# Optimization experiments

Hardware: AMD Instinct MI355X
Metric: run time of the kernel (lower is better)

Reference implementation:

```python
import jax, jax.numpy as jnp
import numpy as np

N, B, C, H = 1024, 4, 1024, 8
D = C // H  # head dim = 128


def setup_inputs() -> dict:
    key = jax.random.key(0)
    ks = jax.random.split(key, 10)
    f = lambda k, s: jax.random.normal(k, s, dtype=jnp.float32)
    w = lambda k: f(k, (C, C)) * 0.02  # torch Linear weight layout (out, in)
    return {
        "query_reg": f(ks[0], (N, B, C)),
        "key_reg": f(ks[1], (N, B, C)),
        "query_cls": f(ks[2], (N, B, C)),
        "key_cls": f(ks[3], (N, B, C)),
        "value": f(ks[4], (N, B, C)),
        "W_q_reg": w(ks[5]),
        "W_k_reg": w(ks[6]),
        "W_q_cls": w(ks[7]),
        "W_k_cls": w(ks[8]),
        "W_v": w(ks[9]),
    }


def _proj_heads(x, W):
    # x: (N, B, C); torch Linear: y = x @ W.T -> reshape (N,B,H,D) -> (B,H,N,D)
    y = jnp.einsum('nbc,dc->nbd', x, W)
    return y.reshape(N, B, H, D).transpose(1, 2, 0, 3)


def _l2norm(x):
    return x / jnp.linalg.norm(x, axis=-1, keepdims=True)


def reference(query_reg, key_reg, query_cls, key_cls, value,
              W_q_reg, W_k_reg, W_q_cls, W_k_cls, W_v):
    q_reg = _l2norm(_proj_heads(query_reg, W_q_reg))  # (B,H,N,D)
    k_reg = _l2norm(_proj_heads(key_reg, W_k_reg))
    q_cls = _l2norm(_proj_heads(query_cls, W_q_cls))
    k_cls = _l2norm(_proj_heads(key_cls, W_k_cls))
    v = _proj_heads(value, W_v)

    attn_reg = jax.nn.softmax(jnp.einsum('bhnd,bhmd->bhnm', q_reg, k_reg), axis=-1)
    attn_cls = jax.nn.softmax(jnp.einsum('bhnd,bhmd->bhnm', q_cls, k_cls), axis=-1)
    attn = (attn_reg + attn_cls) * 0.5  # (B,H,N,N)

    x = jnp.einsum('bhnm,bhmd->bhnd', attn, v)  # (B,H,N,D)
    x = x.transpose(0, 2, 1, 3).reshape(B, N, C)  # (B,N,C)
    return (x.transpose(1, 0, 2), attn)  # ((N,B,C), (B,H,N,N))
```

## Files before the change

### kernel.cpp

```cpp
#include <hip/hip_runtime.h>

#define DEVINL __device__ __forceinline__

typedef unsigned short u16;
typedef float f32x4 __attribute__((ext_vector_type(4)));
typedef __bf16 bf16x8 __attribute__((ext_vector_type(8)));

constexpr int N_ = 1024, B_ = 4, C_ = 1024, H_ = 8, D_ = 128;
constexpr int NB = N_ * B_;
constexpr int BH = B_ * H_;

DEVINL u16 f2bf(float f) {
  unsigned u = __builtin_bit_cast(unsigned, f);
  u += 0x7fffu + ((u >> 16) & 1u);
  return (u16)(u >> 16);
}
DEVINL float bf2f(u16 v) { return __builtin_bit_cast(float, ((unsigned)v) << 16); }

typedef __attribute__((address_space(1))) void gv_t;
typedef __attribute__((address_space(3))) void lv_t;
DEVINL void gload16(const void* g, void* l) {
  __builtin_amdgcn_global_load_lds((gv_t*)(unsigned long long)g,
                                   (lv_t*)(unsigned)(unsigned long long)l, 16, 0, 0);
}
DEVINL bf16x8 ld_frag(const u16* p) { return *(const bf16x8*)p; }
DEVINL f32x4 mfma16(bf16x8 a, bf16x8 b, f32x4 c) {
  return __builtin_amdgcn_mfma_f32_16x16x32_bf16(a, b, c, 0, 0, 0);
}

struct ConvArgs { const float* s[10]; u16* d[10]; int n[10]; };

__global__ __launch_bounds__(256) void k_convert(ConvArgs a) {
  const int which = blockIdx.y;
  const int i = (blockIdx.x * 256 + threadIdx.x) * 8;
  if (i >= a.n[which]) return;
  const float* s = a.s[which] + i;
  float4 v0 = *(const float4*)s;
  float4 v1 = *(const float4*)(s + 4);
  union { uint4 v; u16 r[8]; } u;
  u.r[0] = f2bf(v0.x); u.r[1] = f2bf(v0.y); u.r[2] = f2bf(v0.z); u.r[3] = f2bf(v0.w);
  u.r[4] = f2bf(v1.x); u.r[5] = f2bf(v1.y); u.r[6] = f2bf(v1.z); u.r[7] = f2bf(v1.w);
  *(uint4*)(a.d[which] + i) = u.v;
}

struct ProjArgs { const u16* X[5]; const u16* W[5]; u16* O[5]; };

__global__ __launch_bounds__(256) void k_proj(ProjArgs a) {
  __shared__ u16 lA[128 * 64];
  __shared__ u16 lB[128 * 64];
  __shared__ float lred[128][2];
  const int tid = threadIdx.x, w = tid >> 6, lane = tid & 63;
  const int qd = lane >> 4, m16 = lane & 15;
  const int wr = w >> 1, wc = w & 1;
  const int r0 = blockIdx.y * 128, d0 = blockIdx.x * 128;
  const u16* __restrict__ X = a.X[blockIdx.z];
  const u16* __restrict__ W = a.W[blockIdx.z];
  u16* __restrict__ O = a.O[blockIdx.z];
  const bool donorm = blockIdx.z < 4;

  f32x4 acc[4][4];
  const f32x4 fz = {0.f, 0.f, 0.f, 0.f};
#pragma unroll
  for (int i = 0; i < 4; ++i)
#pragma unroll
    for (int j = 0; j < 4; ++j) acc[i][j] = fz;

  for (int k0 = 0; k0 < C_; k0 += 64) {
    __syncthreads();
#pragma unroll
    for (int i = 0; i < 4; ++i) {
      int p = i * 256 + tid, row = p >> 3, cp = p & 7, cl = cp ^ (row & 7);
      gload16(X + (size_t)(r0 + row) * C_ + k0 + cl * 8, &lA[p * 8]);
    }
#pragma unroll
    for (int i = 0; i < 4; ++i) {
      int p = i * 256 + tid, row = p >> 3, cp = p & 7, cl = cp ^ (row & 7);
      gload16(W + (size_t)(d0 + row) * C_ + k0 + cl * 8, &lB[p * 8]);
    }
    __syncthreads();
#pragma unroll
    for (int ks = 0; ks < 2; ++ks) {
      bf16x8 af[4], bfr[4];
#pragma unroll
      for (int t = 0; t < 4; ++t) {
        int row = wr * 64 + t * 16 + m16;
        af[t] = ld_frag(&lA[row * 64 + (((ks * 4 + qd) ^ (row & 7)) * 8)]);
        int col = wc * 64 + t * 16 + m16;
        bfr[t] = ld_frag(&lB[col * 64 + (((ks * 4 + qd) ^ (col & 7)) * 8)]);
      }
#pragma unroll
      for (int rt = 0; rt < 4; ++rt)
#pragma unroll
        for (int ct = 0; ct < 4; ++ct)
          acc[rt][ct] = mfma16(af[rt], bfr[ct], acc[rt][ct]);
    }
  }
  if (donorm) {
    float s[4][4];
#pragma unroll
    for (int rt = 0; rt < 4; ++rt)
#pragma unroll
      for (int rg = 0; rg < 4; ++rg) {
        float t = 0.f;
#pragma unroll
        for (int ct = 0; ct < 4; ++ct) t += acc[rt][ct][rg] * acc[rt][ct][rg];
        s[rt][rg] = t;
      }
#pragma unroll
    for (int off = 1; off < 16; off <<= 1)
#pragma unroll
      for (int rt = 0; rt < 4; ++rt)
#pragma unroll
        for (int rg = 0; rg < 4; ++rg) s[rt][rg] += __shfl_xor(s[rt][rg], off);
    if (m16 == 0) {
#pragma unroll
      for (int rt = 0; rt < 4; ++rt)
#pragma unroll
        for (int rg = 0; rg < 4; ++rg)
          lred[wr * 64 + rt * 16 + qd * 4 + rg][wc] = s[rt][rg];
    }
  }
  __syncthreads();
  float inv[4][4];
#pragma unroll
  for (int rt = 0; rt < 4; ++rt)
#pragma unroll
    for (int rg = 0; rg < 4; ++rg) {
      if (donorm) {
        int row = wr * 64 + rt * 16 + qd * 4 + rg;
        inv[rt][rg] = rsqrtf(lred[row][0] + lred[row][1]);
      } else inv[rt][rg] = 1.0f;
    }
#pragma unroll
  for (int rt = 0; rt < 4; ++rt)
#pragma unroll
    for (int ct = 0; ct < 4; ++ct)
#pragma unroll
      for (int rg = 0; rg < 4; ++rg) {
        int row = r0 + wr * 64 + rt * 16 + qd * 4 + rg;
        int col = d0 + wc * 64 + ct * 16 + m16;
        int n = row >> 2, b = row & 3, h = col >> 7, d = col & 127;
        O[(((size_t)(b * H_ + h)) * N_ + n) * D_ + d] = f2bf(acc[rt][ct][rg] * inv[rt][rg]);
      }
}

__global__ __launch_bounds__(256) void k_transpose(const u16* __restrict__ v,
                                                   u16* __restrict__ vt) {
  __shared__ u16 tile[128][65];
  const int bh = blockIdx.y, n0 = blockIdx.x * 64;
  const u16* src = v + (size_t)bh * N_ * D_;
  u16* dst = vt + (size_t)bh * D_ * N_;
  union U8 { uint4 v; u16 s[8]; };
#pragma unroll
  for (int it = 0; it < 4; ++it) {
    int c = it * 256 + threadIdx.x;
    int n = c >> 4, dc = (c & 15) * 8;
    U8 u; u.v = *(const uint4*)(src + (size_t)(n0 + n) * D_ + dc);
#pragma unroll
    for (int j = 0; j < 8; ++j) tile[dc + j][n] = u.s[j];
  }
  __syncthreads();
#pragma unroll
  for (int it = 0; it < 4; ++it) {
    int c = it * 256 + threadIdx.x;
    int d = c >> 3, nc = (c & 7) * 8;
    U8 u;
#pragma unroll
    for (int j = 0; j < 8; ++j) u.s[j] = tile[d][nc + j];
    *(uint4*)(dst + (size_t)d * N_ + n0 + nc) = u.v;
  }
}

__global__ __launch_bounds__(256, 2) void k_attn(const u16* __restrict__ qr,
                                                 const u16* __restrict__ kr,
                                                 const u16* __restrict__ qc,
                                                 const u16* __restrict__ kc,
                                                 const u16* __restrict__ vt,
                                                 float* __restrict__ out0,
                                                 float* __restrict__ out1) {
  __shared__ u16 lK[2][128 * 128];
  __shared__ u16 lP[32 * 136];
  __shared__ float lred[2][4][32];
  const int flat = blockIdx.x + (blockIdx.y << 5);
  const int xcd = flat & 7, kk = flat >> 3;
  const int bh = (xcd << 2) + (kk >> 5);
  const int n0 = (kk & 31) * 32;
  const int b = bh >> 3, h = bh & 7;
  const size_t base = (size_t)bh * N_ * D_;
  const int tid = threadIdx.x, w = tid >> 6, lane = tid & 63;
  const int qd = lane >> 4, m16 = lane & 15;

  bf16x8 qf[2][2][4];
#pragma unroll
  for (int ct = 0; ct < 2; ++ct)
#pragma unroll
    for (int ks = 0; ks < 4; ++ks) {
      size_t ro = base + (size_t)(n0 + ct * 16 + m16) * D_ + ks * 32 + qd * 8;
      qf[0][ct][ks] = ld_frag(qr + ro);
      qf[1][ct][ks] = ld_frag(qc + ro);
    }

  uint2 pst[2][8][2][2];
  float psum[2][2] = {{0.f, 0.f}, {0.f, 0.f}};
  const f32x4 fz = {0.f, 0.f, 0.f, 0.f};

#pragma unroll
  for (int mt = 0; mt < 8; ++mt) {
    const int m0 = mt * 128;
    __syncthreads();
#pragma unroll
    for (int i = 0; i < 8; ++i) {
      int p = i * 256 + tid, row = p >> 4, cp = p & 15, cl = cp ^ (row & 15);
      gload16(kr + base + (size_t)(m0 + row) * D_ + cl * 8, &lK[0][p * 8]);
    }
#pragma unroll
    for (int i = 0; i < 8; ++i) {
      int p = i * 256 + tid, row = p >> 4, cp = p & 15, cl = cp ^ (row & 15);
      gload16(kc + base + (size_t)(m0 + row) * D_ + cl * 8, &lK[1][p * 8]);
    }
    __syncthreads();
#pragma unroll
    for (int ty = 0; ty < 2; ++ty) {
#pragma unroll
      for (int rt = 0; rt < 2; ++rt) {
        bf16x8 af[4];
        const int mrow = w * 32 + rt * 16 + m16;
#pragma unroll
        for (int ks = 0; ks < 4; ++ks)
          af[ks] = ld_frag(&lK[ty][mrow * 128 + (((ks * 4 + qd) ^ (mrow & 15)) * 8)]);
#pragma unroll
        for (int ct = 0; ct < 2; ++ct) {
          f32x4 acc = fz;
#pragma unroll
          for (int ks = 0; ks < 4; ++ks) acc = mfma16(af[ks], qf[ty][ct][ks], acc);
          union { uint2 u; u16 s[4]; } pk;
          float loc = 0.f;
#pragma unroll
          for (int rg = 0; rg < 4; ++rg) {
            float e = __expf(acc[rg]);
            loc += e;
            pk.s[rg] = f2bf(e);
          }
          psum[ty][ct] += loc;
          pst[ty][mt][rt][ct] = pk.u;
        }
      }
    }
  }

#pragma unroll
  for (int ty = 0; ty < 2; ++ty)
#pragma unroll
    for (int ct = 0; ct < 2; ++ct) {
      psum[ty][ct] += __shfl_xor(psum[ty][ct], 16);
      psum[ty][ct] += __shfl_xor(psum[ty][ct], 32);
    }
  if (qd == 0) {
#pragma unroll
    for (int ty = 0; ty < 2; ++ty)
#pragma unroll
      for (int ct = 0; ct < 2; ++ct) lred[ty][w][ct * 16 + m16] = psum[ty][ct];
  }
  __syncthreads();
  float il[2][2];
#pragma unroll
  for (int ty = 0; ty < 2; ++ty)
#pragma unroll
    for (int ct = 0; ct < 2; ++ct) {
      int n = ct * 16 + m16;
      il[ty][ct] = 0.5f / (lred[ty][0][n] + lred[ty][1][n] + lred[ty][2][n] + lred[ty][3][n]);
    }

  f32x4 xacc[2][2];
#pragma unroll
  for (int ct = 0; ct < 2; ++ct)
#pragma unroll
    for (int dt = 0; dt < 2; ++dt) xacc[ct][dt] = fz;

  float* attn = out1 + (size_t)bh * N_ * N_;
  const u16* vtb = vt + (size_t)bh * D_ * N_;

#pragma unroll
  for (int mt = 0; mt < 8; ++mt) {
    const int m0 = mt * 128;
    __syncthreads();
#pragma unroll
    for (int rt = 0; rt < 2; ++rt)
#pragma unroll
      for (int ct = 0; ct < 2; ++ct) {
        union { uint2 u; u16 s[4]; } ur, uc, pk;
        ur.u = pst[0][mt][rt][ct];
        uc.u = pst[1][mt][rt][ct];
        f32x4 pv;
#pragma unroll
        for (int rg = 0; rg < 4; ++rg) {
          pv[rg] = bf2f(ur.s[rg]) * il[0][ct] + bf2f(uc.s[rg]) * il[1][ct];
          pk.s[rg] = f2bf(pv[rg]);
        }
        const int nrow = n0 + ct * 16 + m16;
        const int mcol = m0 + w * 32 + rt * 16 + qd * 4;
        *(f32x4*)(attn + (size_t)nrow * N_ + mcol) = pv;
        *(uint2*)&lP[(ct * 16 + m16) * 136 + w * 32 + rt * 16 + qd * 4] = pk.u;
      }
    __syncthreads();
#pragma unroll
    for (int ks = 0; ks < 4; ++ks) {
      bf16x8 pa[2], vb[2];
#pragma unroll
      for (int ct = 0; ct < 2; ++ct)
        pa[ct] = ld_frag(&lP[(ct * 16 + m16) * 136 + ks * 32 + qd * 8]);
#pragma unroll
      for (int dt = 0; dt < 2; ++dt)
        vb[dt] = ld_frag(vtb + (size_t)(w * 32 + dt * 16 + m16) * N_ + m0 + ks * 32 + qd * 8);
#pragma unroll
      for (int ct = 0; ct < 2; ++ct)
#pragma unroll
        for (int dt = 0; dt < 2; ++dt)
          xacc[ct][dt] = mfma16(pa[ct], vb[dt], xacc[ct][dt]);
    }
  }
#pragma unroll
  for (int ct = 0; ct < 2; ++ct)
#pragma unroll
    for (int dt = 0; dt < 2; ++dt)
#pragma unroll
      for (int rg = 0; rg < 4; ++rg) {
        int n = n0 + ct * 16 + qd * 4 + rg;
        int d = w * 32 + dt * 16 + m16;
        out0[((size_t)n * B_ + b) * C_ + h * 128 + d] = xacc[ct][dt][rg];
      }
}

extern "C" void kernel_launch(void* const* d_in, const int* in_sizes, int n_in,
                              void* d_out, int out_size, void* d_ws, size_t ws_size,
                              hipStream_t stream) {
  (void)in_sizes; (void)n_in; (void)out_size; (void)ws_size;
  const float* in_f[10];
  for (int i = 0; i < 10; ++i) in_f[i] = (const float*)d_in[i];

  u16* ws = (u16*)d_ws;
  u16* Xc[5], *Wc[5], *P[5];
  for (int i = 0; i < 5; ++i) Xc[i] = ws + (size_t)i * NB * C_;
  u16* wbase = ws + (size_t)5 * NB * C_;
  for (int i = 0; i < 5; ++i) Wc[i] = wbase + (size_t)i * C_ * C_;
  u16* pbase = wbase + (size_t)5 * C_ * C_;
  for (int i = 0; i < 5; ++i) P[i] = pbase + (size_t)i * BH * N_ * D_;
  u16* vt = pbase + (size_t)5 * BH * N_ * D_;

  float* out0 = (float*)d_out;
  float* out1 = out0 + (size_t)N_ * B_ * C_;

  ConvArgs ca;
  for (int i = 0; i < 5; ++i) { ca.s[i] = in_f[i];     ca.d[i] = Xc[i];  ca.n[i] = NB * C_; }
  for (int i = 0; i < 5; ++i) { ca.s[5+i] = in_f[5+i]; ca.d[5+i] = Wc[i]; ca.n[5+i] = C_ * C_; }
  k_convert<<<dim3(2048, 10), 256, 0, stream>>>(ca);

  ProjArgs pa;
  for (int i = 0; i < 5; ++i) { pa.X[i] = Xc[i]; pa.W[i] = Wc[i]; pa.O[i] = P[i]; }
  k_proj<<<dim3(C_ / 128, NB / 128, 5), 256, 0, stream>>>(pa);

  k_transpose<<<dim3(N_ / 64, BH), 256, 0, stream>>>(P[4], vt);

  k_attn<<<dim3(N_ / 32, BH), 256, 0, stream>>>(P[0], P[1], P[2], P[3], vt, out0, out1);
}
```

Baseline: 411.9 us.

## Double-buffer K tiles and widen attention block to eight waves

The attention kernel now runs 512 threads per block, so each wave handles 16 key rows or 16 head dims instead of 32. The next K tile is prefetched into a second LDS buffer while the current one is used for QK^T, and the P staging buffer is also doubled, which drops one barrier per iteration in the PV loop. The aim is to hide K load latency behind MFMA and exp work and to cut per-thread register pressure. The cost is roughly 145KB of LDS, which limits residency to one block per CU despite the launch bound of two.

```diff
diff --git a/kernel.cpp b/kernel.cpp
--- a/kernel.cpp
+++ b/kernel.cpp
@@ -171,16 +171,16 @@
   }
 }
 
-__global__ __launch_bounds__(256, 2) void k_attn(const u16* __restrict__ qr,
+__global__ __launch_bounds__(512, 2) void k_attn(const u16* __restrict__ qr,
                                                  const u16* __restrict__ kr,
                                                  const u16* __restrict__ qc,
                                                  const u16* __restrict__ kc,
                                                  const u16* __restrict__ vt,
                                                  float* __restrict__ out0,
                                                  float* __restrict__ out1) {
-  __shared__ u16 lK[2][128 * 128];
-  __shared__ u16 lP[32 * 136];
-  __shared__ float lred[2][4][32];
+  __shared__ u16 lK[2][2][128 * 128];
+  __shared__ u16 lP[2][32 * 136];
+  __shared__ float lred[2][8][32];
   const int flat = blockIdx.x + (blockIdx.y << 5);
   const int xcd = flat & 7, kk = flat >> 3;
   const int bh = (xcd << 2) + (kk >> 5);
@@ -189,6 +189,7 @@
   const size_t base = (size_t)bh * N_ * D_;
   const int tid = threadIdx.x, w = tid >> 6, lane = tid & 63;
   const int qd = lane >> 4, m16 = lane & 15;
+  const u16* ksrc[2] = {kr, kc};
 
   bf16x8 qf[2][2][4];
 #pragma unroll
@@ -200,52 +201,58 @@
       qf[1][ct][ks] = ld_frag(qc + ro);
     }
 
-  uint2 pst[2][8][2][2];
+  uint2 pst[2][8][2];
   float psum[2][2] = {{0.f, 0.f}, {0.f, 0.f}};
   const f32x4 fz = {0.f, 0.f, 0.f, 0.f};
 
 #pragma unroll
+  for (int ty = 0; ty < 2; ++ty)
+#pragma unroll
+    for (int i = 0; i < 4; ++i) {
+      int p = i * 512 + tid, row = p >> 4, cp = p & 15, cl = cp ^ (row & 15);
+      gload16(ksrc[ty] + base + (size_t)row * D_ + cl * 8, &lK[0][ty][p * 8]);
+    }
+  __syncthreads();
+
+#pragma unroll
   for (int mt = 0; mt < 8; ++mt) {
-    const int m0 = mt * 128;
+    const int cur = mt & 1;
+    if (mt < 7) {
+      const int m0n = (mt + 1) * 128;
+#pragma unroll
+      for (int ty = 0; ty < 2; ++ty)
+#pragma unroll
+        for (int i = 0; i < 4; ++i) {
+          int p = i * 512 + tid, row = p >> 4, cp = p & 15, cl = cp ^ (row & 15);
+          gload16(ksrc[ty] + base + (size_t)(m0n + row) * D_ + cl * 8,
+                  &lK[cur ^ 1][ty][p * 8]);
+        }
+    }
+    const int mrow = w * 16 + m16;
+#pragma unroll
+    for (int ty = 0; ty < 2; ++ty) {
+      bf16x8 af[4];
+#pragma unroll
+      for (int ks = 0; ks < 4; ++ks)
+        af[ks] = ld_frag(&lK[cur][ty][mrow * 128 + (((ks * 4 + qd) ^ (mrow & 15)) * 8)]);
+#pragma unroll
+      for (int ct = 0; ct < 2; ++ct) {
+        f32x4 acc = fz;
+#pragma unroll
+        for (int ks = 0; ks < 4; ++ks) acc = mfma16(af[ks], qf[ty][ct][ks], acc);
+        union { uint2 u; u16 s[4]; } pk;
+        float loc = 0.f;
+#pragma unroll
+        for (int rg = 0; rg < 4; ++rg) {
+          float e = __expf(acc[rg]);
+          loc += e;
+          pk.s[rg] = f2bf(e);
+        }
+        psum[ty][ct] += loc;
+        pst[ty][mt][ct] = pk.u;
+      }
+    }
     __syncthreads();
-#pragma unroll
-    for (int i = 0; i < 8; ++i) {
-      int p = i * 256 + tid, row = p >> 4, cp = p & 15, cl = cp ^ (row & 15);
-      gload16(kr + base + (size_t)(m0 + row) * D_ + cl * 8, &lK[0][p * 8]);
-    }
-#pragma unroll
-    for (int i = 0; i < 8; ++i) {
-      int p = i * 256 + tid, row = p >> 4, cp = p & 15, cl = cp ^ (row & 15);
-      gload16(kc + base + (size_t)(m0 + row) * D_ + cl * 8, &lK[1][p * 8]);
-    }
-    __syncthreads();
-#pragma unroll
-    for (int ty = 0; ty < 2; ++ty) {
-#pragma unroll
-      for (int rt = 0; rt < 2; ++rt) {
-        bf16x8 af[4];
-        const int mrow = w * 32 + rt * 16 + m16;
-#pragma unroll
-        for (int ks = 0; ks < 4; ++ks)
-          af[ks] = ld_frag(&lK[ty][mrow * 128 + (((ks * 4 + qd) ^ (mrow & 15)) * 8)]);
-#pragma unroll
-        for (int ct = 0; ct < 2; ++ct) {
-          f32x4 acc = fz;
-#pragma unroll
-          for (int ks = 0; ks < 4; ++ks) acc = mfma16(af[ks], qf[ty][ct][ks], acc);
-          union { uint2 u; u16 s[4]; } pk;
-          float loc = 0.f;
-#pragma unroll
-          for (int rg = 0; rg < 4; ++rg) {
-            float e = __expf(acc[rg]);
-            loc += e;
-            pk.s[rg] = f2bf(e);
-          }
-          psum[ty][ct] += loc;
-          pst[ty][mt][rt][ct] = pk.u;
-        }
-      }
-    }
   }
 
 #pragma unroll
@@ -268,67 +275,57 @@
 #pragma unroll
     for (int ct = 0; ct < 2; ++ct) {
       int n = ct * 16 + m16;
-      il[ty][ct] = 0.5f / (lred[ty][0][n] + lred[ty][1][n] + lred[ty][2][n] + lred[ty][3][n]);
-    }
-
-  f32x4 xacc[2][2];
+      float s = 0.f;
+#pragma unroll
+      for (int ww = 0; ww < 8; ++ww) s += lred[ty][ww][n];
+      il[ty][ct] = 0.5f / s;
+    }
+
+  f32x4 xacc[2] = {fz, fz};
+  float* attn = out1 + (size_t)bh * N_ * N_;
+  const u16* vtb = vt + (size_t)bh * D_ * N_ + (size_t)(w * 16 + m16) * N_;
+
+#pragma unroll
+  for (int mt = 0; mt < 8; ++mt) {
+    const int cur = mt & 1;
+    const int m0 = mt * 128;
+#pragma unroll
+    for (int ct = 0; ct < 2; ++ct) {
+      union { uint2 u; u16 s[4]; } ur, uc, pk;
+      ur.u = pst[0][mt][ct];
+      uc.u = pst[1][mt][ct];
+      f32x4 pv;
+#pragma unroll
+      for (int rg = 0; rg < 4; ++rg) {
+        pv[rg] = bf2f(ur.s[rg]) * il[0][ct] + bf2f(uc.s[rg]) * il[1][ct];
+        pk.s[rg] = f2bf(pv[rg]);
+      }
+      const int nrow = n0 + ct * 16 + m16;
+      const int mcol = m0 + w * 16 + qd * 4;
+      *(f32x4*)(attn + (size_t)nrow * N_ + mcol) = pv;
+      *(uint2*)&lP[cur][(ct * 16 + m16) * 136 + w * 16 + qd * 4] = pk.u;
+    }
+    __syncthreads();
+#pragma unroll
+    for (int ks = 0; ks < 4; ++ks) {
+      bf16x8 pa[2];
+#pragma unroll
+      for (int ct = 0; ct < 2; ++ct)
+        pa[ct] = ld_frag(&lP[cur][(ct * 16 + m16) * 136 + ks * 32 + qd * 8]);
+      bf16x8 vb = ld_frag(vtb + m0 + ks * 32 + qd * 8);
+#pragma unroll
+      for (int ct = 0; ct < 2; ++ct)
+        xacc[ct] = mfma16(pa[ct], vb, xacc[ct]);
+    }
+  }
 #pragma unroll
   for (int ct = 0; ct < 2; ++ct)
 #pragma unroll
-    for (int dt = 0; dt < 2; ++dt) xacc[ct][dt] = fz;
-
-  float* attn = out1 + (size_t)bh * N_ * N_;
-  const u16* vtb = vt + (size_t)bh * D_ * N_;
-
-#pragma unroll
-  for (int mt = 0; mt < 8; ++mt) {
-    const int m0 = mt * 128;
-    __syncthreads();
-#pragma unroll
-    for (int rt = 0; rt < 2; ++rt)
-#pragma unroll
-      for (int ct = 0; ct < 2; ++ct) {
-        union { uint2 u; u16 s[4]; } ur, uc, pk;
-        ur.u = pst[0][mt][rt][ct];
-        uc.u = pst[1][mt][rt][ct];
-        f32x4 pv;
-#pragma unroll
-        for (int rg = 0; rg < 4; ++rg) {
-          pv[rg] = bf2f(ur.s[rg]) * il[0][ct] + bf2f(uc.s[rg]) * il[1][ct];
-          pk.s[rg] = f2bf(pv[rg]);
-        }
-        const int nrow = n0 + ct * 16 + m16;
-        const int mcol = m0 + w * 32 + rt * 16 + qd * 4;
-        *(f32x4*)(attn + (size_t)nrow * N_ + mcol) = pv;
-        *(uint2*)&lP[(ct * 16 + m16) * 136 + w * 32 + rt * 16 + qd * 4] = pk.u;
-      }
-    __syncthreads();
-#pragma unroll
-    for (int ks = 0; ks < 4; ++ks) {
-      bf16x8 pa[2], vb[2];
-#pragma unroll
-      for (int ct = 0; ct < 2; ++ct)
-        pa[ct] = ld_frag(&lP[(ct * 16 + m16) * 136 + ks * 32 + qd * 8]);
-#pragma unroll
-      for (int dt = 0; dt < 2; ++dt)
-        vb[dt] = ld_frag(vtb + (size_t)(w * 32 + dt * 16 + m16) * N_ + m0 + ks * 32 + qd * 8);
-#pragma unroll
-      for (int ct = 0; ct < 2; ++ct)
-#pragma unroll
-        for (int dt = 0; dt < 2; ++dt)
-          xacc[ct][dt] = mfma16(pa[ct], vb[dt], xacc[ct][dt]);
-    }
-  }
-#pragma unroll
-  for (int ct = 0; ct < 2; ++ct)
-#pragma unroll
-    for (int dt = 0; dt < 2; ++dt)
-#pragma unroll
-      for (int rg = 0; rg < 4; ++rg) {
-        int n = n0 + ct * 16 + qd * 4 + rg;
-        int d = w * 32 + dt * 16 + m16;
-        out0[((size_t)n * B_ + b) * C_ + h * 128 + d] = xacc[ct][dt][rg];
-      }
+    for (int rg = 0; rg < 4; ++rg) {
+      int n = n0 + ct * 16 + qd * 4 + rg;
+      int d = w * 16 + m16;
+      out0[((size_t)n * B_ + b) * C_ + h * 128 + d] = xacc[ct][rg];
+    }
 }
 
 extern "C" void kernel_launch(void* const* d_in, const int* in_sizes, int n_in,
@@ -361,5 +358,5 @@
 
   k_transpose<<<dim3(N_ / 64, BH), 256, 0, stream>>>(P[4], vt);
 
-  k_attn<<<dim3(N_ / 32, BH), 256, 0, stream>>>(P[0], P[1], P[2], P[3], vt, out0, out1);
-}
+  k_attn<<<dim3(N_ / 32, BH), 512, 0, stream>>>(P[0], P[1], P[2], P[3], vt, out0, out1);
+}
```

After: 392.3 us. -4.8%, faster.
